# Kernel tuning notes

Hardware: AMD Instinct MI355X
Metric: run time of the kernel (lower is better)

The kernel has to match this reference:

```python
import jax, jax.numpy as jnp
import numpy as np

N_NODES = 50000
N_EDGES = 800000
N_GRAPHS = 512
IN_DIM = 50
H = 128  # hidden_channels


def _init_linear(key, out_dim, in_dim, bias=True):
    k1, k2 = jax.random.split(key)
    bound = 1.0 / np.sqrt(in_dim)
    W = jax.random.uniform(k1, (out_dim, in_dim), jnp.float32, -bound, bound)
    if bias:
        b = jax.random.uniform(k2, (out_dim,), jnp.float32, -bound, bound)
        return W, b
    return W


def setup_inputs() -> dict:
    key = jax.random.key(0)
    ks = jax.random.split(key, 16)
    x = jax.random.normal(ks[0], (N_NODES, IN_DIM), jnp.float32)
    edge_index = jax.random.randint(ks[1], (2, N_EDGES), 0, N_NODES, jnp.int64)
    batch = jnp.sort(jax.random.randint(ks[2], (N_NODES,), 0, N_GRAPHS, jnp.int64))
    Wl1, bl1 = _init_linear(ks[3], H, IN_DIM)
    Wr1 = _init_linear(ks[4], H, IN_DIM, bias=False)
    Wl2, bl2 = _init_linear(ks[5], 2 * H, H)
    Wr2 = _init_linear(ks[6], 2 * H, H, bias=False)
    Wl3, bl3 = _init_linear(ks[7], 4 * H, 2 * H)
    Wr3 = _init_linear(ks[8], 4 * H, 2 * H, bias=False)
    Wf1, bf1 = _init_linear(ks[9], 2 * H, 4 * H)
    Wf2, bf2 = _init_linear(ks[10], H, 2 * H)
    Wo, bo = _init_linear(ks[11], 1, H)
    return dict(x=x, edge_index=edge_index, batch=batch,
                Wl1=Wl1, bl1=bl1, Wr1=Wr1,
                Wl2=Wl2, bl2=bl2, Wr2=Wr2,
                Wl3=Wl3, bl3=bl3, Wr3=Wr3,
                Wf1=Wf1, bf1=bf1, Wf2=Wf2, bf2=bf2, Wo=Wo, bo=bo)


def sage_conv(x, src, dst, deg_inv, Wl, bl, Wr):
    # mean-aggregate neighbor features at destination nodes, then linear
    agg = jax.ops.segment_sum(x[src], dst, num_segments=N_NODES) * deg_inv
    return agg @ Wl.T + bl + x @ Wr.T


def reference(x, edge_index, batch, Wl1, bl1, Wr1, Wl2, bl2, Wr2,
              Wl3, bl3, Wr3, Wf1, bf1, Wf2, bf2, Wo, bo):
    src, dst = edge_index[0], edge_index[1]
    deg = jax.ops.segment_sum(jnp.ones((N_EDGES,), x.dtype), dst, num_segments=N_NODES)
    deg_inv = (1.0 / jnp.maximum(deg, 1.0))[:, None]

    x1 = jax.nn.leaky_relu(sage_conv(x, src, dst, deg_inv, Wl1, bl1, Wr1))
    x2 = jax.nn.relu(sage_conv(x1, src, dst, deg_inv, Wl2, bl2, Wr2))
    x3 = jax.nn.relu(sage_conv(x2, src, dst, deg_inv, Wl3, bl3, Wr3))

    # global mean pool per graph
    pool_sum = jax.ops.segment_sum(x3, batch, num_segments=N_GRAPHS)
    cnt = jax.ops.segment_sum(jnp.ones((N_NODES,), x.dtype), batch, num_segments=N_GRAPHS)
    x_pool = pool_sum / jnp.maximum(cnt, 1.0)[:, None]

    x4 = jax.nn.relu(x_pool @ Wf1.T + bf1)
    x5 = jax.nn.relu(x4 @ Wf2.T + bf2)
    return jax.nn.sigmoid(x5 @ Wo.T + bo)
```

## Files before the change

### kernel.cpp

```cpp
#include <hip/hip_runtime.h>
#include <math.h>

#define N_NODES 50000
#define N_EDGES 800000
#define N_GRAPHS 512
#define M_PAD 50048
#define SEG_SZ 6250

typedef unsigned char u8;
typedef unsigned short u16;
typedef unsigned int u32;
typedef long i64;
using floatx4 = __attribute__((ext_vector_type(4))) float;
using floatx2 = __attribute__((ext_vector_type(2))) float;

__device__ __forceinline__ u8 f2fp8(float v) {
    return (u8)(__builtin_amdgcn_cvt_pk_fp8_f32(v, v, 0, false) & 0xFF);
}
__device__ __forceinline__ u32 pack4fp8(float a, float b, float c, float d) {
    u32 p = __builtin_amdgcn_cvt_pk_fp8_f32(a, b, 0, false);
    return __builtin_amdgcn_cvt_pk_fp8_f32(c, d, p, true);
}
__device__ __forceinline__ void acc16fp8(float* acc, uint4 u) {
    const u32 w[4] = {u.x, u.y, u.z, u.w};
    #pragma unroll
    for (int j = 0; j < 4; ++j) {
        floatx2 lo = __builtin_amdgcn_cvt_pk_f32_fp8((int)w[j], false);
        floatx2 hi = __builtin_amdgcn_cvt_pk_f32_fp8((int)w[j], true);
        acc[j * 4 + 0] += lo[0]; acc[j * 4 + 1] += lo[1];
        acc[j * 4 + 2] += hi[0]; acc[j * 4 + 3] += hi[1];
    }
}

__device__ __forceinline__ void load_lds16(const u8* g, u8* l) {
    __builtin_amdgcn_global_load_lds(
        (const __attribute__((address_space(1))) u32*)g,
        (__attribute__((address_space(3))) u32*)l, 16, 0, 0);
}
template<int N> __device__ __forceinline__ void waitcnt_vm() {
    __builtin_amdgcn_s_waitcnt(0x0F70 | N);
}
__device__ __forceinline__ void raw_barrier() {
    asm volatile("s_barrier" ::: "memory");
}

#define EPT 8
__global__ __launch_bounds__(256) void count_seg_kernel(const int* __restrict__ dst,
                                                        int* __restrict__ degi) {
    const int seg = blockIdx.x & 7;
    const int lo = seg * SEG_SZ, hi = lo + SEG_SZ;
    int e = (blockIdx.x >> 3) * (256 * EPT) + threadIdx.x;
    #pragma unroll
    for (int j = 0; j < EPT; ++j, e += 256) {
        if (e < N_EDGES) {
            int d = dst[e];
            if (d >= lo && d < hi) atomicAdd(&degi[d], 1);
        }
    }
}

__global__ __launch_bounds__(256) void fill_seg_kernel(const int* __restrict__ src,
                                                       const int* __restrict__ dst,
                                                       const int* __restrict__ starts,
                                                       int* __restrict__ cursor,
                                                       u16* __restrict__ csr) {
    const int seg = blockIdx.x & 7;
    const int lo = seg * SEG_SZ, hi = lo + SEG_SZ;
    int e = (blockIdx.x >> 3) * (256 * EPT) + threadIdx.x;
    #pragma unroll
    for (int j = 0; j < EPT; ++j, e += 256) {
        if (e < N_EDGES) {
            int d = dst[e];
            if (d >= lo && d < hi) {
                int p = atomicAdd(&cursor[d], 1);
                csr[starts[d] + p] = (u16)src[e];
            }
        }
    }
}

__global__ void scan1_kernel(const int* __restrict__ degi, int* __restrict__ starts,
                             int* __restrict__ bsum) {
    __shared__ int s[256];
    int t = threadIdx.x, i = blockIdx.x * 256 + t;
    int v = (i < N_NODES) ? degi[i] : 0;
    s[t] = v; __syncthreads();
    for (int off = 1; off < 256; off <<= 1) {
        int x = (t >= off) ? s[t - off] : 0;
        __syncthreads();
        s[t] += x;
        __syncthreads();
    }
    if (i < N_NODES) starts[i] = s[t] - v;
    if (t == 255) bsum[blockIdx.x] = s[255];
}

__global__ void scan2_kernel(const int* __restrict__ bsum, int* __restrict__ boff,
                             int* __restrict__ starts, int nb) {
    __shared__ int s[256];
    int t = threadIdx.x;
    int v = (t < nb) ? bsum[t] : 0;
    s[t] = v; __syncthreads();
    for (int off = 1; off < 256; off <<= 1) {
        int x = (t >= off) ? s[t - off] : 0;
        __syncthreads();
        s[t] += x;
        __syncthreads();
    }
    if (t < nb) boff[t] = s[t] - v;
    if (t == nb - 1) starts[N_NODES] = s[t];
}

__global__ void scan3_kernel(int* __restrict__ starts, const int* __restrict__ boff) {
    int i = blockIdx.x * 256 + threadIdx.x;
    if (i < N_NODES) starts[i] += boff[blockIdx.x];
}

__global__ void gstart_kernel(const int* __restrict__ batch, int* __restrict__ gstart) {
    int i = blockIdx.x * blockDim.x + threadIdx.x;
    if (i >= N_NODES) return;
    int b = batch[i];
    int bp = (i == 0) ? -1 : batch[i - 1];
    for (int g = bp + 1; g <= b; ++g) gstart[g] = i;
    if (i == N_NODES - 1)
        for (int g = b + 1; g <= N_GRAPHS; ++g) gstart[g] = N_NODES;
}

__global__ void cntinv_kernel(const int* __restrict__ gstart, float* __restrict__ cntinv) {
    int g = blockIdx.x * blockDim.x + threadIdx.x;
    if (g < N_GRAPHS) cntinv[g] = 1.0f / fmaxf((float)(gstart[g + 1] - gstart[g]), 1.0f);
}

__global__ void conv_x_kernel(const float* __restrict__ x, u8* __restrict__ abuf1) {
    int i = blockIdx.x * blockDim.x + threadIdx.x;
    if (i >= N_NODES * 16) return;
    int n = i >> 4, c = (i & 15) * 4;
    float v[4];
    #pragma unroll
    for (int j = 0; j < 4; ++j) {
        int cc = c + j;
        v[j] = (cc < 50) ? x[n * 50 + cc] : 0.0f;
    }
    *(u32*)(abuf1 + (size_t)n * 128 + 64 + c) = pack4fp8(v[0], v[1], v[2], v[3]);
}

__global__ void conv_w_all_kernel(const float* __restrict__ Wl1, const float* __restrict__ Wr1,
                                  const float* __restrict__ Wl2, const float* __restrict__ Wr2,
                                  const float* __restrict__ Wl3, const float* __restrict__ Wr3,
                                  const float* __restrict__ Wf1, const float* __restrict__ Wf2,
                                  u8* __restrict__ wb1, u8* __restrict__ wb2,
                                  u8* __restrict__ wb3,
                                  float* __restrict__ Wf1T, float* __restrict__ Wf2T) {
    int i = blockIdx.x * blockDim.x + threadIdx.x;
    if (i < 128 * 64) {
        int o = i / 64, c = i % 64;
        float vl = (c < 50) ? Wl1[o * 50 + c] : 0.0f;
        float vr = (c < 50) ? Wr1[o * 50 + c] : 0.0f;
        wb1[(size_t)o * 128 + c] = f2fp8(vl);
        wb1[(size_t)o * 128 + 64 + c] = f2fp8(vr);
        return;
    }
    i -= 128 * 64;
    if (i < 256 * 128) {
        int o = i / 128, c = i % 128;
        wb2[(size_t)o * 256 + c] = f2fp8(Wl2[o * 128 + c]);
        wb2[(size_t)o * 256 + 128 + c] = f2fp8(Wr2[o * 128 + c]);
        return;
    }
    i -= 256 * 128;
    if (i < 512 * 256) {
        int o = i / 256, c = i % 256;
        wb3[(size_t)o * 512 + c] = f2fp8(Wl3[o * 256 + c]);
        wb3[(size_t)o * 512 + 256 + c] = f2fp8(Wr3[o * 256 + c]);
        return;
    }
    i -= 512 * 256;
    if (i < 256 * 512) {
        int o = i >> 9, k = i & 511;
        Wf1T[(size_t)k * 256 + o] = Wf1[(size_t)o * 512 + k];
        return;
    }
    i -= 256 * 512;
    if (i < 128 * 256) {
        int o = i >> 8, k = i & 255;
        Wf2T[(size_t)k * 128 + o] = Wf2[(size_t)o * 256 + k];
    }
}

template<int DINP>
__global__ __launch_bounds__(256) void csr_agg_kernel(const int* __restrict__ starts,
                                                      const u16* __restrict__ csr,
                                                      u8* __restrict__ abuf) {
    constexpr int STRIDE = 2 * DINP;
    constexpr int LPR = DINP / 16;
    constexpr int EPW = 64 / LPR;
    const int wave = threadIdx.x >> 6, lane = threadIdx.x & 63;
    const int n = blockIdx.x * 4 + wave;
    if (n >= N_NODES) return;
    const int sub = lane / LPR;
    const int li = lane % LPR;
    const int s0 = starts[n], s1 = starts[n + 1];

    float acc[16] = {};
    const u8* xin = abuf + DINP;

    int e = s0 + sub;
    for (; e + EPW < s1; e += 2 * EPW) {
        int i0 = csr[e], i1 = csr[e + EPW];
        uint4 u0 = *(const uint4*)(xin + (size_t)i0 * STRIDE + li * 16);
        uint4 u1 = *(const uint4*)(xin + (size_t)i1 * STRIDE + li * 16);
        acc16fp8(acc, u0);
        acc16fp8(acc, u1);
    }
    for (; e < s1; e += EPW) {
        int i0 = csr[e];
        uint4 u0 = *(const uint4*)(xin + (size_t)i0 * STRIDE + li * 16);
        acc16fp8(acc, u0);
    }

    #pragma unroll
    for (int off = 32; off >= LPR; off >>= 1) {
        #pragma unroll
        for (int c = 0; c < 16; ++c) acc[c] += __shfl_down(acc[c], off);
    }

    if (lane < LPR) {
        float sc = 1.0f / fmaxf((float)(s1 - s0), 1.0f);
        uint4 o;
        o.x = pack4fp8(acc[0] * sc, acc[1] * sc, acc[2] * sc, acc[3] * sc);
        o.y = pack4fp8(acc[4] * sc, acc[5] * sc, acc[6] * sc, acc[7] * sc);
        o.z = pack4fp8(acc[8] * sc, acc[9] * sc, acc[10] * sc, acc[11] * sc);
        o.w = pack4fp8(acc[12] * sc, acc[13] * sc, acc[14] * sc, acc[15] * sc);
        *(uint4*)(abuf + (size_t)n * STRIDE + li * 16) = o;
    }
}

template<int K, int NB, int ACT>
__global__ __launch_bounds__(256) void gemm_fp8_kernel(
    const u8* __restrict__ A, const u8* __restrict__ W,
    const float* __restrict__ bias,
    u8* __restrict__ out8, int gstride, int goff, int N)
{
    constexpr int NKB = K / 32;
    constexpr int MT = M_PAD / 128;
    constexpr int MCHUNK = (MT + 7) / 8;
    __shared__ __align__(16) u8 As[3][128 * 32];
    __shared__ __align__(16) u8 Bs[3][128 * 32];

    const int bx = blockIdx.x;
    const int xcd = bx & 7;
    const int seq = bx >> 3;
    const int n = seq % NB;
    const int m = xcd * MCHUNK + seq / NB;
    if (m >= MT) return;
    const int bm = m * 128;
    const int bn = n * 128;

    const int tid = threadIdx.x;
    const int wave = tid >> 6, lane = tid & 63;
    const int wm = (wave & 1) * 64, wn = (wave >> 1) * 64;
    const int lm = lane & 15, lq = lane >> 4;

    const int srow = wave * 32 + (lane >> 1);
    const int scol = ((lane & 1) ^ ((lane >> 3) & 1)) * 16;
    const u8* gA = A + (size_t)(bm + srow) * K + scol;
    const u8* gB = W + (size_t)(bn + srow) * K + scol;
    const int lbase = wave * 32 * 32;

    auto stage = [&](int s, int r) {
        const int ko = s * 32;
        load_lds16(gA + ko, &As[r][lbase]);
        load_lds16(gB + ko, &Bs[r][lbase]);
    };

    floatx4 acc[4][4] = {};

    stage(0, 0);
    stage(1, 1);

    const int csw = (((lq >> 1) ^ ((lm >> 2) & 1)) << 4) + (lq & 1) * 8;

    #pragma unroll
    for (int kb = 0; kb < NKB; ++kb) {
        if (kb + 2 < NKB) stage(kb + 2, (kb + 2) % 3);
        const int rem = NKB - 1 - kb;
        if (rem >= 2)      waitcnt_vm<4>();
        else if (rem == 1) waitcnt_vm<2>();
        else               waitcnt_vm<0>();
        raw_barrier();

        const int r = kb % 3;
        i64 af[4], bfr[4];
        #pragma unroll
        for (int mi = 0; mi < 4; ++mi)
            af[mi] = *(const i64*)&As[r][(wm + mi * 16 + lm) * 32 + csw];
        #pragma unroll
        for (int ni = 0; ni < 4; ++ni)
            bfr[ni] = *(const i64*)&Bs[r][(wn + ni * 16 + lm) * 32 + csw];
        #pragma unroll
        for (int mi = 0; mi < 4; ++mi)
            #pragma unroll
            for (int ni = 0; ni < 4; ++ni)
                acc[mi][ni] = __builtin_amdgcn_mfma_f32_16x16x32_fp8_fp8(
                    af[mi], bfr[ni], acc[mi][ni], 0, 0, 0);
        raw_barrier();
    }

    #pragma unroll
    for (int mi = 0; mi < 4; ++mi) {
        int node0 = bm + wm + mi * 16 + lq * 4;
        #pragma unroll
        for (int ni = 0; ni < 4; ++ni) {
            int o = bn + wn + ni * 16 + lm;
            float bi = bias[o];
            #pragma unroll
            for (int r = 0; r < 4; ++r) {
                int node = node0 + r;
                if (node >= N) continue;
                float v = acc[mi][ni][r] + bi;
                if (ACT == 0) v = (v > 0.0f) ? v : 0.01f * v;
                else          v = fmaxf(v, 0.0f);
                out8[(size_t)node * gstride + goff + o] = f2fp8(v);
            }
        }
    }
}

__global__ __launch_bounds__(256) void pool_kernel(
    const u8* __restrict__ x3, const int* __restrict__ gstart,
    const float* __restrict__ cntinv, float* __restrict__ pool)
{
    __shared__ float sacc[32][128];
    const int g = blockIdx.x >> 2;
    const int slab = blockIdx.x & 3;
    const int t = threadIdx.x;
    const int chain = t >> 3;
    const int li = t & 7;
    const int c0 = slab * 128 + li * 16;
    const int n0 = gstart[g], n1 = gstart[g + 1];

    float acc[16] = {};
    for (int n = n0 + chain; n < n1; n += 32) {
        uint4 u = *(const uint4*)(x3 + (size_t)n * 512 + c0);
        acc16fp8(acc, u);
    }
    #pragma unroll
    for (int j = 0; j < 16; ++j) sacc[chain][li * 16 + j] = acc[j];
    __syncthreads();
    if (t < 128) {
        float s = 0.0f;
        #pragma unroll
        for (int r = 0; r < 32; ++r) s += sacc[r][t];
        pool[(size_t)g * 512 + slab * 128 + t] = s * cntinv[g];
    }
}

__global__ __launch_bounds__(256) void dense_head_kernel(
    const float* __restrict__ pool,
    const float* __restrict__ Wf1T, const float* __restrict__ bf1,
    const float* __restrict__ Wf2T, const float* __restrict__ bf2,
    const float* __restrict__ Wo,  const float* __restrict__ bo,
    float* __restrict__ out)
{
    __shared__ float sp[512];
    __shared__ float s4[256];
    __shared__ float red[128];
    const int g = blockIdx.x;
    const int t = threadIdx.x;

    sp[t]       = pool[(size_t)g * 512 + t];
    sp[t + 256] = pool[(size_t)g * 512 + 256 + t];
    __syncthreads();

    {
        float s = bf1[t];
        #pragma unroll 8
        for (int k = 0; k < 512; ++k) s += sp[k] * Wf1T[(size_t)k * 256 + t];
        s4[t] = fmaxf(s, 0.0f);
    }
    __syncthreads();
    if (t < 128) {
        float s = bf2[t];
        #pragma unroll 8
        for (int k = 0; k < 256; ++k) s += s4[k] * Wf2T[(size_t)k * 128 + t];
        red[t] = fmaxf(s, 0.0f) * Wo[t];
    }
    __syncthreads();
    for (int off = 64; off >= 1; off >>= 1) {
        if (t < off) red[t] += red[t + off];
        __syncthreads();
    }
    if (t == 0) out[g] = 1.0f / (1.0f + expf(-(red[0] + bo[0])));
}

extern "C" void kernel_launch(void* const* d_in, const int* in_sizes, int n_in,
                              void* d_out, int out_size, void* d_ws, size_t ws_size,
                              hipStream_t stream)
{
    const float* x     = (const float*)d_in[0];
    const int*   ei    = (const int*)  d_in[1];
    const int*   batch = (const int*)  d_in[2];
    const float* Wl1   = (const float*)d_in[3];
    const float* bl1   = (const float*)d_in[4];
    const float* Wr1   = (const float*)d_in[5];
    const float* Wl2   = (const float*)d_in[6];
    const float* bl2   = (const float*)d_in[7];
    const float* Wr2   = (const float*)d_in[8];
    const float* Wl3   = (const float*)d_in[9];
    const float* bl3   = (const float*)d_in[10];
    const float* Wr3   = (const float*)d_in[11];
    const float* Wf1   = (const float*)d_in[12];
    const float* bf1   = (const float*)d_in[13];
    const float* Wf2   = (const float*)d_in[14];
    const float* bf2   = (const float*)d_in[15];
    const float* Wo    = (const float*)d_in[16];
    const float* bo    = (const float*)d_in[17];

    const int* src = ei;
    const int* dst = ei + N_EDGES;

    char* p = (char*)d_ws;
    auto alloc = [&](size_t bytes) { char* r = p; p += (bytes + 255) & ~(size_t)255; return r; };
    int*   gstart = (int*)  alloc(513 * 4);
    float* cntinv = (float*)alloc(512 * 4);
    float* pool   = (float*)alloc((size_t)512 * 512 * 4);
    float* Wf1T   = (float*)alloc((size_t)512 * 256 * 4);
    float* Wf2T   = (float*)alloc((size_t)256 * 128 * 4);
    u8*    abuf3  = (u8*)   alloc((size_t)M_PAD * 512);
    u8*    wb3    = (u8*)   alloc((size_t)512 * 512);
    char* ubase = p;
    int*   degi   = (int*)  alloc(50176 * 4);
    int*   cursor = (int*)  alloc(50176 * 4);
    int*   starts = (int*)  alloc(50432 * 4);
    int*   bsum   = (int*)  alloc(256 * 4);
    int*   boff   = (int*)  alloc(256 * 4);
    u16*   csr    = (u16*)  alloc((size_t)N_EDGES * 2);
    u8*    abuf1  = (u8*)   alloc((size_t)M_PAD * 128);
    u8*    abuf2  = (u8*)   alloc((size_t)M_PAD * 256);
    u8*    wb1    = (u8*)   alloc((size_t)128 * 128);
    u8*    wb2    = (u8*)   alloc((size_t)256 * 256);
    u8*    x3buf8 = (u8*)ubase;

    hipMemsetAsync(degi, 0, 2 * 50176 * 4, stream);
    const int SEG_BLOCKS = (N_EDGES + 256 * EPT - 1) / (256 * EPT);
    count_seg_kernel<<<SEG_BLOCKS * 8, 256, 0, stream>>>(dst, degi);
    scan1_kernel<<<196, 256, 0, stream>>>(degi, starts, bsum);
    scan2_kernel<<<1, 256, 0, stream>>>(bsum, boff, starts, 196);
    scan3_kernel<<<196, 256, 0, stream>>>(starts, boff);
    fill_seg_kernel<<<SEG_BLOCKS * 8, 256, 0, stream>>>(src, dst, starts, cursor, csr);
    gstart_kernel<<<196, 256, 0, stream>>>(batch, gstart);
    cntinv_kernel<<<2, 256, 0, stream>>>(gstart, cntinv);

    conv_x_kernel<<<(N_NODES * 16 + 255) / 256, 256, 0, stream>>>(x, abuf1);
    const int CONV_N = 128 * 64 + 256 * 128 + 512 * 256 + 256 * 512 + 128 * 256;
    conv_w_all_kernel<<<(CONV_N + 255) / 256, 256, 0, stream>>>(
        Wl1, Wr1, Wl2, Wr2, Wl3, Wr3, Wf1, Wf2, wb1, wb2, wb3, Wf1T, Wf2T);

    const int GB = 12500;
    const int GEMM_GRID = 49 * 8;

    csr_agg_kernel<64><<<GB, 256, 0, stream>>>(starts, csr, abuf1);
    gemm_fp8_kernel<128, 1, 0><<<GEMM_GRID * 1, 256, 0, stream>>>(
        abuf1, wb1, bl1, abuf2, 256, 128, N_NODES);

    csr_agg_kernel<128><<<GB, 256, 0, stream>>>(starts, csr, abuf2);
    gemm_fp8_kernel<256, 2, 1><<<GEMM_GRID * 2, 256, 0, stream>>>(
        abuf2, wb2, bl2, abuf3, 512, 256, N_NODES);

    csr_agg_kernel<256><<<GB, 256, 0, stream>>>(starts, csr, abuf3);
    gemm_fp8_kernel<512, 4, 1><<<GEMM_GRID * 4, 256, 0, stream>>>(
        abuf3, wb3, bl3, x3buf8, 512, 0, N_NODES);

    pool_kernel<<<N_GRAPHS * 4, 256, 0, stream>>>(x3buf8, gstart, cntinv, pool);
    dense_head_kernel<<<N_GRAPHS, 256, 0, stream>>>(
        pool, Wf1T, bf1, Wf2T, bf2, Wo, bo, (float*)d_out);
}
```

Measured before the change: 385.3 us.

## Fuse global mean pooling into last GEMM epilogue and merge conversion kernels

```diff
diff --git a/kernel.cpp b/kernel.cpp
--- a/kernel.cpp
+++ b/kernel.cpp
@@ -126,32 +126,28 @@
         for (int g = b + 1; g <= N_GRAPHS; ++g) gstart[g] = N_NODES;
 }
 
-__global__ void cntinv_kernel(const int* __restrict__ gstart, float* __restrict__ cntinv) {
-    int g = blockIdx.x * blockDim.x + threadIdx.x;
-    if (g < N_GRAPHS) cntinv[g] = 1.0f / fmaxf((float)(gstart[g + 1] - gstart[g]), 1.0f);
-}
-
-__global__ void conv_x_kernel(const float* __restrict__ x, u8* __restrict__ abuf1) {
+__global__ void conv_all_kernel(const float* __restrict__ x,
+                                const float* __restrict__ Wl1, const float* __restrict__ Wr1,
+                                const float* __restrict__ Wl2, const float* __restrict__ Wr2,
+                                const float* __restrict__ Wl3, const float* __restrict__ Wr3,
+                                const float* __restrict__ Wf1, const float* __restrict__ Wf2,
+                                u8* __restrict__ abuf1,
+                                u8* __restrict__ wb1, u8* __restrict__ wb2,
+                                u8* __restrict__ wb3,
+                                float* __restrict__ Wf1T, float* __restrict__ Wf2T) {
     int i = blockIdx.x * blockDim.x + threadIdx.x;
-    if (i >= N_NODES * 16) return;
-    int n = i >> 4, c = (i & 15) * 4;
-    float v[4];
-    #pragma unroll
-    for (int j = 0; j < 4; ++j) {
-        int cc = c + j;
-        v[j] = (cc < 50) ? x[n * 50 + cc] : 0.0f;
-    }
-    *(u32*)(abuf1 + (size_t)n * 128 + 64 + c) = pack4fp8(v[0], v[1], v[2], v[3]);
-}
-
-__global__ void conv_w_all_kernel(const float* __restrict__ Wl1, const float* __restrict__ Wr1,
-                                  const float* __restrict__ Wl2, const float* __restrict__ Wr2,
-                                  const float* __restrict__ Wl3, const float* __restrict__ Wr3,
-                                  const float* __restrict__ Wf1, const float* __restrict__ Wf2,
-                                  u8* __restrict__ wb1, u8* __restrict__ wb2,
-                                  u8* __restrict__ wb3,
-                                  float* __restrict__ Wf1T, float* __restrict__ Wf2T) {
-    int i = blockIdx.x * blockDim.x + threadIdx.x;
+    if (i < N_NODES * 16) {
+        int n = i >> 4, c = (i & 15) * 4;
+        float v[4];
+        #pragma unroll
+        for (int j = 0; j < 4; ++j) {
+            int cc = c + j;
+            v[j] = (cc < 50) ? x[n * 50 + cc] : 0.0f;
+        }
+        *(u32*)(abuf1 + (size_t)n * 128 + 64 + c) = pack4fp8(v[0], v[1], v[2], v[3]);
+        return;
+    }
+    i -= N_NODES * 16;
     if (i < 128 * 64) {
         int o = i / 64, c = i % 64;
         float vl = (c < 50) ? Wl1[o * 50 + c] : 0.0f;
@@ -235,11 +231,12 @@
     }
 }
 
-template<int K, int NB, int ACT>
+template<int K, int NB, int ACT, int MODE>
 __global__ __launch_bounds__(256) void gemm_fp8_kernel(
     const u8* __restrict__ A, const u8* __restrict__ W,
     const float* __restrict__ bias,
-    u8* __restrict__ out8, int gstride, int goff, int N)
+    u8* __restrict__ out8, int gstride, int goff,
+    float* __restrict__ pool, const int* __restrict__ batch, int N)
 {
     constexpr int NKB = K / 32;
     constexpr int MT = M_PAD / 128;
@@ -306,57 +303,90 @@
         raw_barrier();
     }
 
-    #pragma unroll
-    for (int mi = 0; mi < 4; ++mi) {
-        int node0 = bm + wm + mi * 16 + lq * 4;
-        #pragma unroll
-        for (int ni = 0; ni < 4; ++ni) {
-            int o = bn + wn + ni * 16 + lm;
-            float bi = bias[o];
+    if constexpr (MODE == 1) {
+        __shared__ float pool_l[8][128];
+        const int nhi = (bm + 127 < N) ? bm + 127 : N - 1;
+        const int g_lo = batch[bm];
+        const int g_hi = batch[nhi];
+        const int span = g_hi - g_lo + 1;
+        const bool fast = (span <= 8);
+        if (fast) {
+            for (int i = tid; i < 8 * 128; i += 256) ((float*)pool_l)[i] = 0.0f;
+        }
+        __syncthreads();
+        #pragma unroll
+        for (int mi = 0; mi < 4; ++mi) {
+            int node0 = bm + wm + mi * 16 + lq * 4;
+            int b0 = (node0 < N) ? batch[node0] : -1;
+            int b3 = (node0 + 3 < N) ? batch[node0 + 3] : -2;
             #pragma unroll
-            for (int r = 0; r < 4; ++r) {
-                int node = node0 + r;
-                if (node >= N) continue;
-                float v = acc[mi][ni][r] + bi;
-                if (ACT == 0) v = (v > 0.0f) ? v : 0.01f * v;
-                else          v = fmaxf(v, 0.0f);
-                out8[(size_t)node * gstride + goff + o] = f2fp8(v);
+            for (int ni = 0; ni < 4; ++ni) {
+                int oc = wn + ni * 16 + lm;
+                float bi = bias[bn + oc];
+                float v[4];
+                #pragma unroll
+                for (int r = 0; r < 4; ++r) {
+                    int node = node0 + r;
+                    v[r] = (node < N) ? fmaxf(acc[mi][ni][r] + bi, 0.0f) : 0.0f;
+                }
+                if (fast) {
+                    if (b0 == b3) {
+                        atomicAdd(&pool_l[b0 - g_lo][oc], v[0] + v[1] + v[2] + v[3]);
+                    } else {
+                        #pragma unroll
+                        for (int r = 0; r < 4; ++r) {
+                            int node = node0 + r;
+                            if (node < N)
+                                atomicAdd(&pool_l[batch[node] - g_lo][oc], v[r]);
+                        }
+                    }
+                } else {
+                    if (b0 == b3) {
+                        atomicAdd(&pool[(size_t)b0 * 512 + bn + oc],
+                                  v[0] + v[1] + v[2] + v[3]);
+                    } else {
+                        for (int r = 0; r < 4; ++r) {
+                            int node = node0 + r;
+                            if (node < N)
+                                atomicAdd(&pool[(size_t)batch[node] * 512 + bn + oc], v[r]);
+                        }
+                    }
+                }
             }
         }
-    }
-}
-
-__global__ __launch_bounds__(256) void pool_kernel(
-    const u8* __restrict__ x3, const int* __restrict__ gstart,
-    const float* __restrict__ cntinv, float* __restrict__ pool)
-{
-    __shared__ float sacc[32][128];
-    const int g = blockIdx.x >> 2;
-    const int slab = blockIdx.x & 3;
-    const int t = threadIdx.x;
-    const int chain = t >> 3;
-    const int li = t & 7;
-    const int c0 = slab * 128 + li * 16;
-    const int n0 = gstart[g], n1 = gstart[g + 1];
-
-    float acc[16] = {};
-    for (int n = n0 + chain; n < n1; n += 32) {
-        uint4 u = *(const uint4*)(x3 + (size_t)n * 512 + c0);
-        acc16fp8(acc, u);
-    }
-    #pragma unroll
-    for (int j = 0; j < 16; ++j) sacc[chain][li * 16 + j] = acc[j];
-    __syncthreads();
-    if (t < 128) {
-        float s = 0.0f;
-        #pragma unroll
-        for (int r = 0; r < 32; ++r) s += sacc[r][t];
-        pool[(size_t)g * 512 + slab * 128 + t] = s * cntinv[g];
+        __syncthreads();
+        if (fast) {
+            for (int i = tid; i < span * 128; i += 256) {
+                int gg = i >> 7, cc = i & 127;
+                float val = pool_l[gg][cc];
+                if (val != 0.0f)
+                    atomicAdd(&pool[(size_t)(g_lo + gg) * 512 + bn + cc], val);
+            }
+        }
+    } else {
+        #pragma unroll
+        for (int mi = 0; mi < 4; ++mi) {
+            int node0 = bm + wm + mi * 16 + lq * 4;
+            #pragma unroll
+            for (int ni = 0; ni < 4; ++ni) {
+                int o = bn + wn + ni * 16 + lm;
+                float bi = bias[o];
+                #pragma unroll
+                for (int r = 0; r < 4; ++r) {
+                    int node = node0 + r;
+                    if (node >= N) continue;
+                    float v = acc[mi][ni][r] + bi;
+                    if (ACT == 0) v = (v > 0.0f) ? v : 0.01f * v;
+                    else          v = fmaxf(v, 0.0f);
+                    out8[(size_t)node * gstride + goff + o] = f2fp8(v);
+                }
+            }
+        }
     }
 }
 
 __global__ __launch_bounds__(256) void dense_head_kernel(
-    const float* __restrict__ pool,
+    const float* __restrict__ pool, const int* __restrict__ gstart,
     const float* __restrict__ Wf1T, const float* __restrict__ bf1,
     const float* __restrict__ Wf2T, const float* __restrict__ bf2,
     const float* __restrict__ Wo,  const float* __restrict__ bo,
@@ -367,9 +397,10 @@
     __shared__ float red[128];
     const int g = blockIdx.x;
     const int t = threadIdx.x;
-
-    sp[t]       = pool[(size_t)g * 512 + t];
-    sp[t + 256] = pool[(size_t)g * 512 + 256 + t];
+    const float sc = 1.0f / fmaxf((float)(gstart[g + 1] - gstart[g]), 1.0f);
+
+    sp[t]       = pool[(size_t)g * 512 + t] * sc;
+    sp[t + 256] = pool[(size_t)g * 512 + 256 + t] * sc;
     __syncthreads();
 
     {
@@ -422,26 +453,25 @@
     char* p = (char*)d_ws;
     auto alloc = [&](size_t bytes) { char* r = p; p += (bytes + 255) & ~(size_t)255; return r; };
     int*   gstart = (int*)  alloc(513 * 4);
-    float* cntinv = (float*)alloc(512 * 4);
-    float* pool   = (float*)alloc((size_t)512 * 512 * 4);
     float* Wf1T   = (float*)alloc((size_t)512 * 256 * 4);
     float* Wf2T   = (float*)alloc((size_t)256 * 128 * 4);
+    u8*    abuf1  = (u8*)   alloc((size_t)M_PAD * 128);
+    u8*    abuf2  = (u8*)   alloc((size_t)M_PAD * 256);
     u8*    abuf3  = (u8*)   alloc((size_t)M_PAD * 512);
+    u8*    wb1    = (u8*)   alloc((size_t)128 * 128);
+    u8*    wb2    = (u8*)   alloc((size_t)256 * 256);
     u8*    wb3    = (u8*)   alloc((size_t)512 * 512);
-    char* ubase = p;
+    char*  zbase  = p;
     int*   degi   = (int*)  alloc(50176 * 4);
     int*   cursor = (int*)  alloc(50176 * 4);
+    float* pool   = (float*)alloc((size_t)512 * 512 * 4);
+    size_t zbytes = (size_t)(p - zbase);
     int*   starts = (int*)  alloc(50432 * 4);
     int*   bsum   = (int*)  alloc(256 * 4);
     int*   boff   = (int*)  alloc(256 * 4);
     u16*   csr    = (u16*)  alloc((size_t)N_EDGES * 2);
-    u8*    abuf1  = (u8*)   alloc((size_t)M_PAD * 128);
-    u8*    abuf2  = (u8*)   alloc((size_t)M_PAD * 256);
-    u8*    wb1    = (u8*)   alloc((size_t)128 * 128);
-    u8*    wb2    = (u8*)   alloc((size_t)256 * 256);
-    u8*    x3buf8 = (u8*)ubase;
-
-    hipMemsetAsync(degi, 0, 2 * 50176 * 4, stream);
+
+    hipMemsetAsync(zbase, 0, zbytes, stream);
     const int SEG_BLOCKS = (N_EDGES + 256 * EPT - 1) / (256 * EPT);
     count_seg_kernel<<<SEG_BLOCKS * 8, 256, 0, stream>>>(dst, degi);
     scan1_kernel<<<196, 256, 0, stream>>>(degi, starts, bsum);
@@ -449,29 +479,28 @@
     scan3_kernel<<<196, 256, 0, stream>>>(starts, boff);
     fill_seg_kernel<<<SEG_BLOCKS * 8, 256, 0, stream>>>(src, dst, starts, cursor, csr);
     gstart_kernel<<<196, 256, 0, stream>>>(batch, gstart);
-    cntinv_kernel<<<2, 256, 0, stream>>>(gstart, cntinv);
-
-    conv_x_kernel<<<(N_NODES * 16 + 255) / 256, 256, 0, stream>>>(x, abuf1);
-    const int CONV_N = 128 * 64 + 256 * 128 + 512 * 256 + 256 * 512 + 128 * 256;
-    conv_w_all_kernel<<<(CONV_N + 255) / 256, 256, 0, stream>>>(
-        Wl1, Wr1, Wl2, Wr2, Wl3, Wr3, Wf1, Wf2, wb1, wb2, wb3, Wf1T, Wf2T);
+
+    const int CONV_N = N_NODES * 16 + 128 * 64 + 256 * 128 + 512 * 256
+                     + 256 * 512 + 128 * 256;
+    conv_all_kernel<<<(CONV_N + 255) / 256, 256, 0, stream>>>(
+        x, Wl1, Wr1, Wl2, Wr2, Wl3, Wr3, Wf1, Wf2,
+        abuf1, wb1, wb2, wb3, Wf1T, Wf2T);
 
     const int GB = 12500;
     const int GEMM_GRID = 49 * 8;
 
     csr_agg_kernel<64><<<GB, 256, 0, stream>>>(starts, csr, abuf1);
-    gemm_fp8_kernel<128, 1, 0><<<GEMM_GRID * 1, 256, 0, stream>>>(
-        abuf1, wb1, bl1, abuf2, 256, 128, N_NODES);
+    gemm_fp8_kernel<128, 1, 0, 0><<<GEMM_GRID * 1, 256, 0, stream>>>(
+        abuf1, wb1, bl1, abuf2, 256, 128, nullptr, nullptr, N_NODES);
 
     csr_agg_kernel<128><<<GB, 256, 0, stream>>>(starts, csr, abuf2);
-    gemm_fp8_kernel<256, 2, 1><<<GEMM_GRID * 2, 256, 0, stream>>>(
-        abuf2, wb2, bl2, abuf3, 512, 256, N_NODES);
+    gemm_fp8_kernel<256, 2, 1, 0><<<GEMM_GRID * 2, 256, 0, stream>>>(
+        abuf2, wb2, bl2, abuf3, 512, 256, nullptr, nullptr, N_NODES);
 
     csr_agg_kernel<256><<<GB, 256, 0, stream>>>(starts, csr, abuf3);
-    gemm_fp8_kernel<512, 4, 1><<<GEMM_GRID * 4, 256, 0, stream>>>(
-        abuf3, wb3, bl3, x3buf8, 512, 0, N_NODES);
-
-    pool_kernel<<<N_GRAPHS * 4, 256, 0, stream>>>(x3buf8, gstart, cntinv, pool);
+    gemm_fp8_kernel<512, 4, 1, 1><<<GEMM_GRID * 4, 256, 0, stream>>>(
+        abuf3, wb3, bl3, nullptr, 0, 0, pool, batch, N_NODES);
+
     dense_head_kernel<<<N_GRAPHS, 256, 0, stream>>>(
-        pool, Wf1T, bf1, Wf2T, bf2, Wo, bo, (float*)d_out);
-}
+        pool, gstart, Wf1T, bf1, Wf2T, bf2, Wo, bo, (float*)d_out);
+}
```

Result: slower. 405.6 us (+5.3%).
